# Performance work log

Measured on AMD Instinct MI355X. Metric: run time of the kernel, lower is better.

## Reference

```python
import jax, jax.numpy as jnp
import numpy as np
import math

NUM_HEADS = 8


def _dwconv(x, w, b, pad):
    # depthwise conv: x (B,C,H,W), w (C,1,k,k)
    c = x.shape[1]
    y = jax.lax.conv_general_dilated(
        x, w, window_strides=(1, 1), padding=[(pad, pad), (pad, pad)],
        feature_group_count=c, dimension_numbers=("NCHW", "OIHW", "NCHW"))
    return y + b[None, :, None, None]


def _conv(x, w, b, pad):
    y = jax.lax.conv_general_dilated(
        x, w, window_strides=(1, 1), padding=[(pad, pad), (pad, pad)],
        dimension_numbers=("NCHW", "OIHW", "NCHW"))
    return y + b[None, :, None, None]


def setup_inputs() -> dict:
    key = jax.random.key(0)
    ks = jax.random.split(key, 6)
    B, C, H, W = 8, 128, 128, 128
    x = jax.random.normal(ks[0], (B, C, H, W), dtype=jnp.float32)
    wq = jax.random.normal(ks[1], (C, 1, 9, 9), dtype=jnp.float32) * 0.05
    wk = jax.random.normal(ks[2], (C, 1, 9, 9), dtype=jnp.float32) * 0.05
    wv = jax.random.normal(ks[3], (C, 1, 9, 9), dtype=jnp.float32) * 0.05
    wo = jax.random.normal(ks[4], (C, C, 3, 3), dtype=jnp.float32) * 0.02
    bq = jnp.zeros((C,), jnp.float32)
    bk = jnp.zeros((C,), jnp.float32)
    bv = jnp.zeros((C,), jnp.float32)
    bo = jnp.zeros((C,), jnp.float32)
    return {"x": x, "wq": wq, "bq": bq, "wk": wk, "bk": bk,
            "wv": wv, "bv": bv, "wo": wo, "bo": bo}


def reference(x, wq, bq, wk, bk, wv, bv, wo, bo):
    b, c, h, w = x.shape
    hds = NUM_HEADS
    d = (h * w) // hds  # spatial dim split across heads
    q = _dwconv(x, wq, bq, 4).reshape(b, c, hds, d).transpose(0, 2, 1, 3)  # (b,hds,c,d)
    k = _dwconv(x, wk, bk, 4).reshape(b, c, hds, d).transpose(0, 2, 3, 1)  # (b,hds,d,c)
    v = _dwconv(x, wv, bv, 4).reshape(b, c, hds, d).transpose(0, 2, 1, 3)  # (b,hds,c,d)
    # channel attention: C x C scores per head, fp32 softmax
    qk = jnp.einsum("bhcd,bhde->bhce", q.astype(jnp.float32), k.astype(jnp.float32)) / math.sqrt(h * w)
    a = jnp.einsum("bhce,bhed->bhcd", jax.nn.softmax(qk, axis=-1), v.astype(jnp.float32))
    a = a.transpose(0, 2, 1, 3).reshape(b, c, h, w)
    return _conv(a, wo, bo, 1)
```

## Files before the change

kernel.cpp:

```cpp
#include <hip/hip_runtime.h>

#define BATCH 8
#define CH 128
#define HH 128
#define WW 128
#define HWSZ 16384
#define NHEADS 8
#define DHEAD 2048

typedef short bf16x8 __attribute__((ext_vector_type(8)));
typedef short bf16x4v __attribute__((ext_vector_type(4)));
typedef float f32x4 __attribute__((ext_vector_type(4)));
typedef float f32x2 __attribute__((ext_vector_type(2)));

static __device__ inline unsigned short f2bf(float f) {
    unsigned u = __builtin_bit_cast(unsigned, f);
    u += 0x7fff + ((u >> 16) & 1);
    return (unsigned short)(u >> 16);
}

__global__ __launch_bounds__(256) void dwconv_qkv_kernel(
    const float* __restrict__ x,
    const float* __restrict__ wq, const float* __restrict__ bq,
    const float* __restrict__ wk, const float* __restrict__ bk,
    const float* __restrict__ wv, const float* __restrict__ bv,
    unsigned short* __restrict__ Qb, unsigned short* __restrict__ Kb,
    unsigned short* __restrict__ Vb)
{
    const int blk  = blockIdx.x;
    const int tile = blk & 3;
    const int bc   = blk >> 2;
    const int b    = bc >> 7;
    const int c    = bc & (CH - 1);
    const int ty0  = (tile >> 1) << 6;
    const int tx0  = (tile & 1) << 6;

    __shared__ float sm[72][76];
    const float* xp = x + (size_t)bc * HWSZ;
    const int tid = threadIdx.x;
    for (int i = tid; i < 1296; i += 256) {
        const int r  = i / 18;
        const int c4 = (i - r * 18) << 2;
        const int gy = ty0 + r - 4;
        const int gx = tx0 + c4 - 4;
        float4 v = make_float4(0.f, 0.f, 0.f, 0.f);
        if ((unsigned)gy < HH && (unsigned)gx < WW)
            v = *(const float4*)&xp[gy * WW + gx];
        *(float4*)&sm[r][c4] = v;
    }
    __syncthreads();

    const float* wqp = wq + c * 81;
    const float* wkp = wk + c * 81;
    const float* wvp = wv + c * 81;

    const int tx  = tid & 15;
    const int ty  = tid >> 4;
    const int x0  = tx << 2;
    const int oy0 = ty << 2;

    f32x2 aq[4][2], ak[4][2], av[4][2];
    const float bqv = bq[c], bkv = bk[c], bvv = bv[c];
    #pragma unroll
    for (int yy = 0; yy < 4; ++yy)
        #pragma unroll
        for (int h = 0; h < 2; ++h) {
            aq[yy][h] = (f32x2){bqv, bqv};
            ak[yy][h] = (f32x2){bkv, bkv};
            av[yy][h] = (f32x2){bvv, bvv};
        }

    #pragma unroll
    for (int r = 0; r < 12; ++r) {
        const float4* rp = (const float4*)&sm[oy0 + r][x0];
        const float4 v0 = rp[0], v1 = rp[1], v2 = rp[2];
        const float vals[12] = {v0.x, v0.y, v0.z, v0.w, v1.x, v1.y, v1.z, v1.w,
                                v2.x, v2.y, v2.z, v2.w};
        #pragma unroll
        for (int dx = 0; dx < 9; ++dx) {
            const f32x2 xa = {vals[dx + 0], vals[dx + 1]};
            const f32x2 xb = {vals[dx + 2], vals[dx + 3]};
            #pragma unroll
            for (int yy = 0; yy < 4; ++yy) {
                const int dy = r - yy;
                if (dy < 0 || dy > 8) continue;
                const float wqv = wqp[dy * 9 + dx];
                const float wkv = wkp[dy * 9 + dx];
                const float wvv = wvp[dy * 9 + dx];
                const f32x2 wq2 = {wqv, wqv}, wk2 = {wkv, wkv}, wv2 = {wvv, wvv};
                aq[yy][0] = __builtin_elementwise_fma(xa, wq2, aq[yy][0]);
                aq[yy][1] = __builtin_elementwise_fma(xb, wq2, aq[yy][1]);
                ak[yy][0] = __builtin_elementwise_fma(xa, wk2, ak[yy][0]);
                ak[yy][1] = __builtin_elementwise_fma(xb, wk2, ak[yy][1]);
                av[yy][0] = __builtin_elementwise_fma(xa, wv2, av[yy][0]);
                av[yy][1] = __builtin_elementwise_fma(xb, wv2, av[yy][1]);
            }
        }
    }

    #pragma unroll
    for (int yy = 0; yy < 4; ++yy) {
        const int y = ty0 + oy0 + yy;
        const size_t off = ((size_t)(b * 8 + (y >> 4)) * CH + c) * DHEAD
                         + (size_t)(y & 15) * WW + tx0 + x0;
        bf16x4v hq, hk, hv;
        hq[0] = (short)f2bf(aq[yy][0][0]); hq[1] = (short)f2bf(aq[yy][0][1]);
        hq[2] = (short)f2bf(aq[yy][1][0]); hq[3] = (short)f2bf(aq[yy][1][1]);
        hk[0] = (short)f2bf(ak[yy][0][0]); hk[1] = (short)f2bf(ak[yy][0][1]);
        hk[2] = (short)f2bf(ak[yy][1][0]); hk[3] = (short)f2bf(ak[yy][1][1]);
        hv[0] = (short)f2bf(av[yy][0][0]); hv[1] = (short)f2bf(av[yy][0][1]);
        hv[2] = (short)f2bf(av[yy][1][0]); hv[3] = (short)f2bf(av[yy][1][1]);
        *(bf16x4v*)&Qb[off] = hq;
        *(bf16x4v*)&Kb[off] = hk;
        *(bf16x4v*)&Vb[off] = hv;
    }
}

__global__ __launch_bounds__(256) void qk_mfma_kernel(
    const unsigned short* __restrict__ Qb, const unsigned short* __restrict__ Kb,
    float* __restrict__ Spart)
{
    const int blk   = blockIdx.x;
    const int split = blk & 7;
    const int bh    = blk >> 3;
    const int t0    = split * 256;

    __shared__ unsigned short Qs[128][72];
    __shared__ unsigned short Ks[128][72];

    const int tid  = threadIdx.x;
    const int wave = tid >> 6;
    const int lane = tid & 63;
    const int lx   = lane & 15;
    const int qd   = lane >> 4;
    const int m0   = (wave & 1) * 64;
    const int n0   = (wave >> 1) * 64;

    f32x4 acc[4][4];
    #pragma unroll
    for (int mi = 0; mi < 4; ++mi)
        #pragma unroll
        for (int ni = 0; ni < 4; ++ni) acc[mi][ni] = (f32x4){0.f, 0.f, 0.f, 0.f};

    const unsigned short* Qp = Qb + (size_t)bh * CH * DHEAD;
    const unsigned short* Kp = Kb + (size_t)bh * CH * DHEAD;

    #pragma unroll 1
    for (int tc = 0; tc < 256; tc += 64) {
        __syncthreads();
        for (int i = tid; i < 1024; i += 256) {
            const int r  = i >> 3;
            const int cl = (i & 7) << 3;
            *(bf16x8*)&Qs[r][cl] = *(const bf16x8*)&Qp[(size_t)r * DHEAD + t0 + tc + cl];
            *(bf16x8*)&Ks[r][cl] = *(const bf16x8*)&Kp[(size_t)r * DHEAD + t0 + tc + cl];
        }
        __syncthreads();
        #pragma unroll
        for (int ki = 0; ki < 2; ++ki) {
            const int kc = ki * 32 + qd * 8;
            bf16x8 a[4], bv[4];
            #pragma unroll
            for (int mi = 0; mi < 4; ++mi)
                a[mi] = *(const bf16x8*)&Qs[m0 + mi * 16 + lx][kc];
            #pragma unroll
            for (int ni = 0; ni < 4; ++ni)
                bv[ni] = *(const bf16x8*)&Ks[n0 + ni * 16 + lx][kc];
            #pragma unroll
            for (int mi = 0; mi < 4; ++mi)
                #pragma unroll
                for (int ni = 0; ni < 4; ++ni)
                    acc[mi][ni] = __builtin_amdgcn_mfma_f32_16x16x32_bf16(
                        a[mi], bv[ni], acc[mi][ni], 0, 0, 0);
        }
    }
    float* Sp = Spart + ((size_t)split * 64 + bh) * (CH * CH);
    #pragma unroll
    for (int mi = 0; mi < 4; ++mi)
        #pragma unroll
        for (int r = 0; r < 4; ++r) {
            const int c = m0 + mi * 16 + qd * 4 + r;
            #pragma unroll
            for (int ni = 0; ni < 4; ++ni)
                Sp[c * CH + n0 + ni * 16 + lx] = acc[mi][ni][r];
        }
}

__global__ __launch_bounds__(256) void softmax_kernel(
    const float* __restrict__ Spart, unsigned short* __restrict__ Pb)
{
    const int row  = blockIdx.x * 4 + (threadIdx.x >> 6);
    const int lane = threadIdx.x & 63;
    float v0 = 0.f, v1 = 0.f;
    #pragma unroll
    for (int s = 0; s < 8; ++s) {
        const float* Sp = Spart + (size_t)s * 64 * CH * CH + (size_t)row * CH;
        v0 += Sp[lane];
        v1 += Sp[lane + 64];
    }
    v0 *= 0.0078125f; v1 *= 0.0078125f;
    float m = fmaxf(v0, v1);
    #pragma unroll
    for (int off = 32; off > 0; off >>= 1) m = fmaxf(m, __shfl_down(m, off));
    m = __shfl(m, 0);
    const float e0 = __expf(v0 - m);
    const float e1 = __expf(v1 - m);
    float s = e0 + e1;
    #pragma unroll
    for (int off = 32; off > 0; off >>= 1) s += __shfl_down(s, off);
    s = __shfl(s, 0);
    const float inv = 1.f / s;
    Pb[(size_t)row * CH + lane]      = f2bf(e0 * inv);
    Pb[(size_t)row * CH + lane + 64] = f2bf(e1 * inv);
}

__global__ __launch_bounds__(256) void pv_mfma_kernel(
    const unsigned short* __restrict__ Pb, const unsigned short* __restrict__ Vb,
    unsigned short* __restrict__ At)
{
    const int blk = blockIdx.x;
    const int t0  = (blk & 15) << 7;
    const int bh  = blk >> 4;

    __shared__ __align__(16) char smem[69632];
    unsigned short (*Ps)[136] = (unsigned short(*)[136])smem;
    unsigned short (*Vs)[136] = (unsigned short(*)[136])(smem + 34816);
    float (*So)[132] = (float(*)[132])smem;

    const int tid  = threadIdx.x;
    const int wave = tid >> 6;
    const int lane = tid & 63;
    const int lx   = lane & 15;
    const int qd   = lane >> 4;
    const int m0   = (wave & 1) * 64;
    const int n0   = (wave >> 1) * 64;

    const unsigned short* Pp = Pb + (size_t)bh * CH * CH;
    const unsigned short* Vp = Vb + (size_t)bh * CH * DHEAD;

    for (int i = tid; i < 2048; i += 256) {
        const int r  = i >> 4;
        const int cl = (i & 15) << 3;
        *(bf16x8*)&Ps[r][cl] = *(const bf16x8*)&Pp[(size_t)r * CH + cl];
    }
    for (int i = tid; i < 2048; i += 256) {
        const int e   = i & 127;
        const int tc8 = (i >> 7) << 3;
        const bf16x8 vv = *(const bf16x8*)&Vp[(size_t)e * DHEAD + t0 + tc8];
        #pragma unroll
        for (int j = 0; j < 8; ++j) Vs[tc8 + j][e] = (unsigned short)vv[j];
    }
    __syncthreads();

    f32x4 acc[4][4];
    #pragma unroll
    for (int mi = 0; mi < 4; ++mi)
        #pragma unroll
        for (int ni = 0; ni < 4; ++ni) acc[mi][ni] = (f32x4){0.f, 0.f, 0.f, 0.f};

    #pragma unroll
    for (int ki = 0; ki < 4; ++ki) {
        const int kc = ki * 32 + qd * 8;
        bf16x8 a[4], bv[4];
        #pragma unroll
        for (int mi = 0; mi < 4; ++mi)
            a[mi] = *(const bf16x8*)&Ps[m0 + mi * 16 + lx][kc];
        #pragma unroll
        for (int ni = 0; ni < 4; ++ni)
            bv[ni] = *(const bf16x8*)&Vs[n0 + ni * 16 + lx][kc];
        #pragma unroll
        for (int mi = 0; mi < 4; ++mi)
            #pragma unroll
            for (int ni = 0; ni < 4; ++ni)
                acc[mi][ni] = __builtin_amdgcn_mfma_f32_16x16x32_bf16(
                    a[mi], bv[ni], acc[mi][ni], 0, 0, 0);
    }

    __syncthreads();
    #pragma unroll
    for (int mi = 0; mi < 4; ++mi)
        #pragma unroll
        for (int ni = 0; ni < 4; ++ni)
            #pragma unroll
            for (int r = 0; r < 4; ++r)
                So[n0 + ni * 16 + lx][m0 + mi * 16 + qd * 4 + r] = acc[mi][ni][r];
    __syncthreads();

    const int t  = tid >> 1;
    const int ch = (tid & 1) * 64;
    const size_t orow = (((size_t)(bh >> 3) * HWSZ) + (size_t)(bh & 7) * DHEAD + t0 + t) * CH + ch;
    #pragma unroll
    for (int j = 0; j < 8; ++j) {
        const float4 f0 = *(const float4*)&So[t][ch + j * 8];
        const float4 f1 = *(const float4*)&So[t][ch + j * 8 + 4];
        bf16x8 h;
        h[0] = (short)f2bf(f0.x); h[1] = (short)f2bf(f0.y);
        h[2] = (short)f2bf(f0.z); h[3] = (short)f2bf(f0.w);
        h[4] = (short)f2bf(f1.x); h[5] = (short)f2bf(f1.y);
        h[6] = (short)f2bf(f1.z); h[7] = (short)f2bf(f1.w);
        *(bf16x8*)&At[orow + j * 8] = h;
    }
}

__global__ __launch_bounds__(256) void wprep_kernel(
    const float* __restrict__ wo, unsigned short* __restrict__ Wt)
{
    const int i = blockIdx.x * 256 + threadIdx.x;
    const int tap = i >> 14;
    const int rem = i & 16383;
    const int co  = rem >> 7;
    const int ci  = rem & 127;
    Wt[i] = f2bf(wo[(size_t)(co * CH + ci) * 9 + tap]);
}

__global__ __launch_bounds__(256, 3) void conv3x3_mfma_kernel(
    const unsigned short* __restrict__ At, const unsigned short* __restrict__ Wt,
    const float* __restrict__ bo, float* __restrict__ out)
{
    const int blk = blockIdx.x;
    const int y   = blk & (HH - 1);
    const int b   = blk >> 7;

    __shared__ unsigned short sA[130][136];
    __shared__ unsigned short sW[128][72];

    const int tid  = threadIdx.x;
    const int wave = tid >> 6;
    const int lane = tid & 63;
    const int lx   = lane & 15;
    const int qd   = lane >> 4;
    const int m0   = (wave & 1) * 64;
    const int n0   = (wave >> 1) * 64;

    for (int i = tid; i < 272; i += 256) {
        const int r   = (i < 136) ? 0 : 129;
        const int col = (i < 136) ? i : (i - 136);
        sA[r][col] = 0;
    }

    f32x4 acc[4][4];
    #pragma unroll
    for (int mi = 0; mi < 4; ++mi) {
        f32x4 bv;
        #pragma unroll
        for (int r = 0; r < 4; ++r) bv[r] = bo[m0 + mi * 16 + qd * 4 + r];
        #pragma unroll
        for (int ni = 0; ni < 4; ++ni) acc[mi][ni] = bv;
    }

    const size_t abase = (size_t)b * HWSZ * CH;

    for (int dy = 0; dy < 3; ++dy) {
        const int gy = y + dy - 1;
        __syncthreads();
        if ((unsigned)gy < HH) {
            const unsigned short* row = At + abase + (size_t)gy * WW * CH;
            for (int i = tid; i < 2048; i += 256) {
                const int xx  = i >> 4;
                const int cc8 = (i & 15) << 3;
                *(float4*)&sA[xx + 1][cc8] = *(const float4*)&row[xx * CH + cc8];
            }
        } else {
            const float4 z = make_float4(0.f, 0.f, 0.f, 0.f);
            for (int i = tid; i < 2048; i += 256) {
                const int xx  = i >> 4;
                const int cc8 = (i & 15) << 3;
                *(float4*)&sA[xx + 1][cc8] = z;
            }
        }
        for (int dx = 0; dx < 3; ++dx) {
            const int tap = dy * 3 + dx;
            #pragma unroll 1
            for (int kh = 0; kh < 2; ++kh) {
                if (dx | kh) __syncthreads();
                const unsigned short* wt = Wt + (size_t)tap * CH * CH + kh * 64;
                for (int i = tid; i < 1024; i += 256) {
                    const int co  = i >> 3;
                    const int cc8 = (i & 7) << 3;
                    *(float4*)&sW[co][cc8] = *(const float4*)&wt[co * CH + cc8];
                }
                __syncthreads();
                #pragma unroll
                for (int ks = 0; ks < 2; ++ks) {
                    const int kc  = ks * 32 + qd * 8;
                    const int kca = kh * 64 + kc;
                    bf16x8 a[4], bfr[4];
                    #pragma unroll
                    for (int mi = 0; mi < 4; ++mi)
                        a[mi] = *(const bf16x8*)&sW[m0 + mi * 16 + lx][kc];
                    #pragma unroll
                    for (int ni = 0; ni < 4; ++ni)
                        bfr[ni] = *(const bf16x8*)&sA[n0 + ni * 16 + lx + dx][kca];
                    #pragma unroll
                    for (int mi = 0; mi < 4; ++mi)
                        #pragma unroll
                        for (int ni = 0; ni < 4; ++ni)
                            acc[mi][ni] = __builtin_amdgcn_mfma_f32_16x16x32_bf16(
                                a[mi], bfr[ni], acc[mi][ni], 0, 0, 0);
                }
            }
        }
    }

    const size_t obase = (size_t)b * CH * HWSZ + (size_t)y * WW;
    #pragma unroll
    for (int mi = 0; mi < 4; ++mi) {
        #pragma unroll
        for (int r = 0; r < 4; ++r) {
            const int co = m0 + mi * 16 + qd * 4 + r;
            float* orow = out + obase + (size_t)co * HWSZ;
            #pragma unroll
            for (int ni = 0; ni < 4; ++ni)
                orow[n0 + ni * 16 + lx] = acc[mi][ni][r];
        }
    }
}

extern "C" void kernel_launch(void* const* d_in, const int* in_sizes, int n_in,
                              void* d_out, int out_size, void* d_ws, size_t ws_size,
                              hipStream_t stream)
{
    const float* x  = (const float*)d_in[0];
    const float* wq = (const float*)d_in[1];
    const float* bq = (const float*)d_in[2];
    const float* wk = (const float*)d_in[3];
    const float* bk = (const float*)d_in[4];
    const float* wv = (const float*)d_in[5];
    const float* bv = (const float*)d_in[6];
    const float* wo = (const float*)d_in[7];
    const float* bo = (const float*)d_in[8];

    char* ws = (char*)d_ws;
    unsigned short* Qb    = (unsigned short*)(ws);
    unsigned short* Kb    = (unsigned short*)(ws + (size_t)33554432);
    unsigned short* Vb    = (unsigned short*)(ws + (size_t)67108864);
    float*          Spart = (float*)        (ws + (size_t)100663296);
    unsigned short* Pb    = (unsigned short*)(ws + (size_t)134217728);
    unsigned short* At    = (unsigned short*)(ws + (size_t)136314880);
    unsigned short* Wt    = (unsigned short*)(ws + (size_t)169869312);

    dwconv_qkv_kernel<<<BATCH * CH * 4, 256, 0, stream>>>(x, wq, bq, wk, bk, wv, bv, Qb, Kb, Vb);
    wprep_kernel<<<576, 256, 0, stream>>>(wo, Wt);
    qk_mfma_kernel<<<64 * 8, 256, 0, stream>>>(Qb, Kb, Spart);
    softmax_kernel<<<2048, 256, 0, stream>>>(Spart, Pb);
    pv_mfma_kernel<<<64 * 16, 256, 0, stream>>>(Pb, Vb, At);
    conv3x3_mfma_kernel<<<BATCH * HH, 256, 0, stream>>>(At, Wt, bo, (float*)d_out);
}
```

Measured before the change: 322.2 us.

## Compute depthwise 9x9 QKV convolution with MFMA via Toeplitz weight matrices

```diff
diff --git a/kernel.cpp b/kernel.cpp
--- a/kernel.cpp
+++ b/kernel.cpp
@@ -12,6 +12,8 @@
 typedef short bf16x4v __attribute__((ext_vector_type(4)));
 typedef float f32x4 __attribute__((ext_vector_type(4)));
 typedef float f32x2 __attribute__((ext_vector_type(2)));
+typedef _Float16 f16x8 __attribute__((ext_vector_type(8)));
+typedef _Float16 f16x4 __attribute__((ext_vector_type(4)));
 
 static __device__ inline unsigned short f2bf(float f) {
     unsigned u = __builtin_bit_cast(unsigned, f);
@@ -19,100 +21,111 @@
     return (unsigned short)(u >> 16);
 }
 
-__global__ __launch_bounds__(256) void dwconv_qkv_kernel(
+__global__ __launch_bounds__(256) void toeplitz_prep_kernel(
+    const float* __restrict__ wq, const float* __restrict__ wk,
+    const float* __restrict__ wv, _Float16* __restrict__ Tp)
+{
+    const int g = blockIdx.x * 256 + threadIdx.x;
+    const int c    = g / 1728;
+    const int rem  = g - c * 1728;
+    const int m    = rem >> 6;
+    const int lane = rem & 63;
+    const int conv = m / 9;
+    const int dy   = m - conv * 9;
+    const float* w = (conv == 0) ? wq : ((conv == 1) ? wk : wv);
+    const int j    = lane & 15;
+    const int kb   = (lane >> 4) << 3;
+    f16x8 h;
+    #pragma unroll
+    for (int e = 0; e < 8; ++e) {
+        const int d = kb + e - j;
+        h[e] = (d >= 0 && d <= 8) ? (_Float16)w[c * 81 + dy * 9 + d]
+                                  : (_Float16)0.f;
+    }
+    *(f16x8*)&Tp[(size_t)g * 8] = h;
+}
+
+__global__ __launch_bounds__(256) void dwconv_qkv_mfma_kernel(
     const float* __restrict__ x,
-    const float* __restrict__ wq, const float* __restrict__ bq,
-    const float* __restrict__ wk, const float* __restrict__ bk,
-    const float* __restrict__ wv, const float* __restrict__ bv,
+    const float* __restrict__ bq, const float* __restrict__ bk,
+    const float* __restrict__ bv,
+    const _Float16* __restrict__ Tp,
     unsigned short* __restrict__ Qb, unsigned short* __restrict__ Kb,
     unsigned short* __restrict__ Vb)
 {
-    const int blk  = blockIdx.x;
-    const int tile = blk & 3;
-    const int bc   = blk >> 2;
-    const int b    = bc >> 7;
-    const int c    = bc & (CH - 1);
-    const int ty0  = (tile >> 1) << 6;
-    const int tx0  = (tile & 1) << 6;
-
-    __shared__ float sm[72][76];
+    const int bc = blockIdx.x;
+    const int b  = bc >> 7;
+    const int c  = bc & (CH - 1);
+
+    __shared__ _Float16 img[136][144];
+
+    const int tid  = threadIdx.x;
+    const int wave = tid >> 6;
+    const int lane = tid & 63;
+    const int lx   = lane & 15;
+    const int qd   = lane >> 4;
+
+    f16x8 Btp[27];
+    const _Float16* tp = Tp + (size_t)c * 13824 + (size_t)lane * 8;
+    #pragma unroll
+    for (int m = 0; m < 27; ++m)
+        Btp[m] = *(const f16x8*)(tp + (size_t)m * 512);
+
+    {
+        f16x8 z = {0, 0, 0, 0, 0, 0, 0, 0};
+        _Float16* flat = &img[0][0];
+        for (int i = tid; i < 2448; i += 256)
+            *(f16x8*)&flat[i * 8] = z;
+    }
+    __syncthreads();
     const float* xp = x + (size_t)bc * HWSZ;
-    const int tid = threadIdx.x;
-    for (int i = tid; i < 1296; i += 256) {
-        const int r  = i / 18;
-        const int c4 = (i - r * 18) << 2;
-        const int gy = ty0 + r - 4;
-        const int gx = tx0 + c4 - 4;
-        float4 v = make_float4(0.f, 0.f, 0.f, 0.f);
-        if ((unsigned)gy < HH && (unsigned)gx < WW)
-            v = *(const float4*)&xp[gy * WW + gx];
-        *(float4*)&sm[r][c4] = v;
+    for (int i = tid; i < 4096; i += 256) {
+        const float4 v = *(const float4*)&xp[i * 4];
+        const int y  = i >> 5;
+        const int xc = (i & 31) << 2;
+        f16x4 h = {(_Float16)v.x, (_Float16)v.y, (_Float16)v.z, (_Float16)v.w};
+        *(f16x4*)&img[y + 4][xc + 4] = h;
     }
     __syncthreads();
 
-    const float* wqp = wq + c * 81;
-    const float* wkp = wk + c * 81;
-    const float* wvp = wv + c * 81;
-
-    const int tx  = tid & 15;
-    const int ty  = tid >> 4;
-    const int x0  = tx << 2;
-    const int oy0 = ty << 2;
-
-    f32x2 aq[4][2], ak[4][2], av[4][2];
     const float bqv = bq[c], bkv = bk[c], bvv = bv[c];
-    #pragma unroll
-    for (int yy = 0; yy < 4; ++yy)
-        #pragma unroll
-        for (int h = 0; h < 2; ++h) {
-            aq[yy][h] = (f32x2){bqv, bqv};
-            ak[yy][h] = (f32x2){bkv, bkv};
-            av[yy][h] = (f32x2){bvv, bvv};
-        }
-
-    #pragma unroll
-    for (int r = 0; r < 12; ++r) {
-        const float4* rp = (const float4*)&sm[oy0 + r][x0];
-        const float4 v0 = rp[0], v1 = rp[1], v2 = rp[2];
-        const float vals[12] = {v0.x, v0.y, v0.z, v0.w, v1.x, v1.y, v1.z, v1.w,
-                                v2.x, v2.y, v2.z, v2.w};
-        #pragma unroll
-        for (int dx = 0; dx < 9; ++dx) {
-            const f32x2 xa = {vals[dx + 0], vals[dx + 1]};
-            const f32x2 xb = {vals[dx + 2], vals[dx + 3]};
-            #pragma unroll
-            for (int yy = 0; yy < 4; ++yy) {
-                const int dy = r - yy;
-                if (dy < 0 || dy > 8) continue;
-                const float wqv = wqp[dy * 9 + dx];
-                const float wkv = wkp[dy * 9 + dx];
-                const float wvv = wvp[dy * 9 + dx];
-                const f32x2 wq2 = {wqv, wqv}, wk2 = {wkv, wkv}, wv2 = {wvv, wvv};
-                aq[yy][0] = __builtin_elementwise_fma(xa, wq2, aq[yy][0]);
-                aq[yy][1] = __builtin_elementwise_fma(xb, wq2, aq[yy][1]);
-                ak[yy][0] = __builtin_elementwise_fma(xa, wk2, ak[yy][0]);
-                ak[yy][1] = __builtin_elementwise_fma(xb, wk2, ak[yy][1]);
-                av[yy][0] = __builtin_elementwise_fma(xa, wv2, av[yy][0]);
-                av[yy][1] = __builtin_elementwise_fma(xb, wv2, av[yy][1]);
-            }
-        }
-    }
-
-    #pragma unroll
-    for (int yy = 0; yy < 4; ++yy) {
-        const int y = ty0 + oy0 + yy;
-        const size_t off = ((size_t)(b * 8 + (y >> 4)) * CH + c) * DHEAD
-                         + (size_t)(y & 15) * WW + tx0 + x0;
-        bf16x4v hq, hk, hv;
-        hq[0] = (short)f2bf(aq[yy][0][0]); hq[1] = (short)f2bf(aq[yy][0][1]);
-        hq[2] = (short)f2bf(aq[yy][1][0]); hq[3] = (short)f2bf(aq[yy][1][1]);
-        hk[0] = (short)f2bf(ak[yy][0][0]); hk[1] = (short)f2bf(ak[yy][0][1]);
-        hk[2] = (short)f2bf(ak[yy][1][0]); hk[3] = (short)f2bf(ak[yy][1][1]);
-        hv[0] = (short)f2bf(av[yy][0][0]); hv[1] = (short)f2bf(av[yy][0][1]);
-        hv[2] = (short)f2bf(av[yy][1][0]); hv[3] = (short)f2bf(av[yy][1][1]);
-        *(bf16x4v*)&Qb[off] = hq;
-        *(bf16x4v*)&Kb[off] = hk;
-        *(bf16x4v*)&Vb[off] = hv;
+
+    #pragma unroll 1
+    for (int t = 0; t < 8; ++t) {
+        const int sg = t * 4 + wave;
+        const int yg = sg >> 2;
+        const int y0 = yg << 4;
+        const int x0 = (sg & 3) << 5;
+
+        f32x4 aq0 = {bqv, bqv, bqv, bqv}, aq1 = aq0;
+        f32x4 ak0 = {bkv, bkv, bkv, bkv}, ak1 = ak0;
+        f32x4 av0 = {bvv, bvv, bvv, bvv}, av1 = av0;
+
+        const _Float16* rp = &img[y0 + lx][x0 + (qd << 3)];
+        #pragma unroll
+        for (int dy = 0; dy < 9; ++dy) {
+            const f16x8 a0 = *(const f16x8*)rp;
+            const f16x8 a1 = *(const f16x8*)(rp + 16);
+            rp += 144;
+            aq0 = __builtin_amdgcn_mfma_f32_16x16x32_f16(a0, Btp[dy],      aq0, 0, 0, 0);
+            aq1 = __builtin_amdgcn_mfma_f32_16x16x32_f16(a1, Btp[dy],      aq1, 0, 0, 0);
+            ak0 = __builtin_amdgcn_mfma_f32_16x16x32_f16(a0, Btp[9 + dy],  ak0, 0, 0, 0);
+            ak1 = __builtin_amdgcn_mfma_f32_16x16x32_f16(a1, Btp[9 + dy],  ak1, 0, 0, 0);
+            av0 = __builtin_amdgcn_mfma_f32_16x16x32_f16(a0, Btp[18 + dy], av0, 0, 0, 0);
+            av1 = __builtin_amdgcn_mfma_f32_16x16x32_f16(a1, Btp[18 + dy], av1, 0, 0, 0);
+        }
+
+        const size_t base = ((size_t)(b * 8 + yg) * CH + c) * DHEAD
+                          + (size_t)(qd << 2) * WW + x0 + lx;
+        #pragma unroll
+        for (int r = 0; r < 4; ++r) {
+            Qb[base + r * WW]      = f2bf(aq0[r]);
+            Qb[base + r * WW + 16] = f2bf(aq1[r]);
+            Kb[base + r * WW]      = f2bf(ak0[r]);
+            Kb[base + r * WW + 16] = f2bf(ak1[r]);
+            Vb[base + r * WW]      = f2bf(av0[r]);
+            Vb[base + r * WW + 16] = f2bf(av1[r]);
+        }
     }
 }
 
@@ -437,8 +450,10 @@
     unsigned short* Pb    = (unsigned short*)(ws + (size_t)134217728);
     unsigned short* At    = (unsigned short*)(ws + (size_t)136314880);
     unsigned short* Wt    = (unsigned short*)(ws + (size_t)169869312);
-
-    dwconv_qkv_kernel<<<BATCH * CH * 4, 256, 0, stream>>>(x, wq, bq, wk, bk, wv, bv, Qb, Kb, Vb);
+    _Float16*       Tp    = (_Float16*)      (ws + (size_t)100663296);
+
+    toeplitz_prep_kernel<<<864, 256, 0, stream>>>(wq, wk, wv, Tp);
+    dwconv_qkv_mfma_kernel<<<BATCH * CH, 256, 0, stream>>>(x, bq, bk, bv, Tp, Qb, Kb, Vb);
     wprep_kernel<<<576, 256, 0, stream>>>(wo, Wt);
     qk_mfma_kernel<<<64 * 8, 256, 0, stream>>>(Qb, Kb, Spart);
     softmax_kernel<<<2048, 256, 0, stream>>>(Spart, Pb);
```

New measurement: 291.4 us. -9.5%, faster.
